# Optimization experiments

Hardware: AMD Instinct MI355X
Metric: run time of the kernel (lower is better)

## Reference

```python
import jax, jax.numpy as jnp
import numpy as np

D_MODEL = 256
D_CONV = 4
EXPAND = 2
D_INNER = EXPAND * D_MODEL  # 512


def silu(v):
    return v * jax.nn.sigmoid(v)


def setup_inputs() -> dict:
    key = jax.random.key(0)
    k0, k1, k2, k3, k4 = jax.random.split(key, 5)
    B, H, W = 4, 128, 128
    x = jax.random.normal(k0, (B, H, W, D_MODEL), jnp.float32)
    # nn.Linear(d_model, 2*d_inner, bias=False) -> weight (2*d_inner, d_model)
    W_in = jax.random.normal(k1, (2 * D_INNER, D_MODEL), jnp.float32) * 0.02
    # depthwise nn.Conv1d(d_inner, d_inner, k=4, groups=d_inner) -> weight (d_inner, 1, k)
    conv_w = jax.random.normal(k2, (D_INNER, 1, D_CONV), jnp.float32) * 0.1
    conv_b = jax.random.normal(k3, (D_INNER,), jnp.float32) * 0.02
    # nn.Linear(d_inner, d_model, bias=False) -> weight (d_model, d_inner)
    W_out = jax.random.normal(k4, (D_MODEL, D_INNER), jnp.float32) * 0.02
    return {"x": x, "W_in": W_in, "conv_w": conv_w, "conv_b": conv_b, "W_out": W_out}


def reference(x, W_in, conv_w, conv_b, W_out):
    B, H, W, C = x.shape
    L = H * W
    x_flat = x.reshape(B, L, C)
    xz = jnp.einsum('blc,dc->bld', x_flat, W_in)         # (B, L, 2*d_inner)
    x_branch, z_branch = jnp.split(xz, 2, axis=-1)
    # depthwise conv1d with padding=d_conv-1 then truncate to L == left-pad by d_conv-1
    u = jax.lax.conv_general_dilated(
        x_branch.transpose(0, 2, 1),                      # (B, D, L)
        conv_w,                                           # (D, 1, K)
        window_strides=(1,),
        padding=[(D_CONV - 1, 0)],
        dimension_numbers=('NCH', 'OIH', 'NCH'),
        feature_group_count=D_INNER,
    )
    u = (u + conv_b[None, :, None]).transpose(0, 2, 1)    # (B, L, D)
    u = silu(u)
    # selective_scan in the source is a stub that returns its input unchanged,
    # so the four directional passes reduce to identity transforms of u.
    y1 = u
    y2 = jnp.flip(jnp.flip(u, axis=1), axis=1)
    u_t = u.reshape(B, H, W, -1).transpose(0, 2, 1, 3).reshape(B, L, -1)
    y3 = u_t.reshape(B, W, H, -1).transpose(0, 2, 1, 3).reshape(B, L, -1)
    y4 = jnp.flip(jnp.flip(u_t, axis=1), axis=1).reshape(B, W, H, -1).transpose(0, 2, 1, 3).reshape(B, L, -1)
    y = (y1 + y2 + y3 + y4) * silu(z_branch)
    out = jnp.einsum('bld,cd->blc', y, W_out)
    return out.reshape(B, H, W, C)
```

## Files before the change

kernel.cpp:

```cpp
#include <hip/hip_runtime.h>

#define LSEQ   16384
#define NBATCH 4
#define BLROWS 65536
#define DM     256
#define DI     512
#define DXZ    1024

#define BM 128
#define BN 128
#define BK 64

typedef __attribute__((ext_vector_type(8))) short s16x8;
typedef __attribute__((ext_vector_type(4))) short s16x4;
typedef __attribute__((ext_vector_type(4))) float f32x4;

__device__ __forceinline__ float bf2f(unsigned short h) {
  union { unsigned u; float f; } c; c.u = ((unsigned)h) << 16; return c.f;
}
__device__ __forceinline__ unsigned short f2bf(float f) {
  union { float f; unsigned u; } c; c.f = f;
  unsigned u = c.u;
  return (unsigned short)((u + 0x7fffu + ((u >> 16) & 1u)) >> 16);
}

__global__ __launch_bounds__(256)
void cvt_f32_bf16(const float* __restrict__ src, unsigned short* __restrict__ dst, int n4) {
  for (int i = blockIdx.x * blockDim.x + threadIdx.x; i < n4; i += gridDim.x * blockDim.x) {
    const float4 v = reinterpret_cast<const float4*>(src)[i];
    s16x4 o;
    o[0] = (short)f2bf(v.x);
    o[1] = (short)f2bf(v.y);
    o[2] = (short)f2bf(v.z);
    o[3] = (short)f2bf(v.w);
    reinterpret_cast<s16x4*>(dst)[i] = o;
  }
}

__device__ __forceinline__ void gload16(const void* g, void* l) {
  __builtin_amdgcn_global_load_lds((__attribute__((address_space(1))) void*)(g),
                                   (__attribute__((address_space(3))) void*)(l),
                                   16, 0, 0);
}

template<int OUT_BF16>
__global__ __launch_bounds__(256, 2)
void gemm_bt(const unsigned short* __restrict__ A,
             const unsigned short* __restrict__ B,
             void* __restrict__ Cv,
             int M, int N, int K) {
  __shared__ unsigned short lds[2][BM * BK + BN * BK];

  const int tid  = threadIdx.x;
  const int lane = tid & 63;
  const int wv   = tid >> 6;
  const int wr   = wv >> 1;
  const int wc   = wv & 1;
  const int m0   = blockIdx.y * BM;
  const int n0   = blockIdx.x * BN;

  const int srow = tid >> 3;
  const int scol = (tid & 7) * 8;

  const int kSteps = K / BK;

  f32x4 acc[4][4];
#pragma unroll
  for (int i = 0; i < 4; ++i)
#pragma unroll
    for (int j = 0; j < 4; ++j)
#pragma unroll
      for (int r = 0; r < 4; ++r) acc[i][j][r] = 0.f;

  auto stage = [&](int ks, int buf) {
    const unsigned short* Ag = A + (size_t)(m0 + srow) * K + ks * BK + scol;
    const unsigned short* Bg = B + (size_t)(n0 + srow) * K + ks * BK + scol;
    unsigned short* lA = &lds[buf][0]       + tid * 8;
    unsigned short* lB = &lds[buf][BM * BK] + tid * 8;
#pragma unroll
    for (int i = 0; i < 4; ++i) {
      gload16(Ag + (size_t)(i * 32) * K, lA + i * 2048);
      gload16(Bg + (size_t)(i * 32) * K, lB + i * 2048);
    }
  };

  stage(0, 0);

  for (int ks = 0; ks < kSteps; ++ks) {
    const int cur = ks & 1;
    __syncthreads();
    if (ks + 1 < kSteps) stage(ks + 1, cur ^ 1);

    const unsigned short* lA = &lds[cur][0];
    const unsigned short* lB = &lds[cur][BM * BK];
    const int lrow = lane & 15;
#pragma unroll
    for (int kk = 0; kk < BK; kk += 32) {
      const int lk = kk + ((lane >> 4) << 3);
      s16x8 af[4], bf[4];
#pragma unroll
      for (int i = 0; i < 4; ++i)
        af[i] = *(const s16x8*)(lA + (wr * 64 + i * 16 + lrow) * BK + lk);
#pragma unroll
      for (int j = 0; j < 4; ++j)
        bf[j] = *(const s16x8*)(lB + (wc * 64 + j * 16 + lrow) * BK + lk);
#pragma unroll
      for (int i = 0; i < 4; ++i)
#pragma unroll
        for (int j = 0; j < 4; ++j)
          acc[i][j] = __builtin_amdgcn_mfma_f32_16x16x32_bf16(af[i], bf[j], acc[i][j], 0, 0, 0);
    }
  }

  const int r0 = (lane >> 4) * 4;
  const int c0 = lane & 15;
  if (OUT_BF16) {
    unsigned short* C = (unsigned short*)Cv;
#pragma unroll
    for (int i = 0; i < 4; ++i)
#pragma unroll
      for (int j = 0; j < 4; ++j) {
        const int rr = m0 + wr * 64 + i * 16 + r0;
        const int cc = n0 + wc * 64 + j * 16 + c0;
#pragma unroll
        for (int r = 0; r < 4; ++r)
          C[(size_t)(rr + r) * N + cc] = f2bf(acc[i][j][r]);
      }
  } else {
    float* C = (float*)Cv;
#pragma unroll
    for (int i = 0; i < 4; ++i)
#pragma unroll
      for (int j = 0; j < 4; ++j) {
        const int rr = m0 + wr * 64 + i * 16 + r0;
        const int cc = n0 + wc * 64 + j * 16 + c0;
#pragma unroll
        for (int r = 0; r < 4; ++r)
          C[(size_t)(rr + r) * N + cc] = acc[i][j][r];
      }
  }
}

__global__ __launch_bounds__(256)
void conv_gate(const unsigned short* __restrict__ xz,
               const float* __restrict__ cw,
               const float* __restrict__ cb,
               unsigned short* __restrict__ y) {
  const int tid      = threadIdx.x;
  const int rowLocal = tid >> 6;
  const int row      = blockIdx.x * 4 + rowLocal;
  const int l        = row & (LSEQ - 1);
  const int d0       = (tid & 63) * 8;
  const size_t base  = (size_t)row * DXZ;

  s16x8 t[4];
#pragma unroll
  for (int k = 0; k < 4; ++k) {
    const int lp = l - 3 + k;
    if (lp >= 0) {
      t[k] = *(const s16x8*)(xz + base + (long)(k - 3) * (long)DXZ + d0);
    } else {
#pragma unroll
      for (int j = 0; j < 8; ++j) t[k][j] = 0;
    }
  }
  const s16x8 zv = *(const s16x8*)(xz + base + DI + d0);

  s16x8 o;
#pragma unroll
  for (int j = 0; j < 8; ++j) {
    const float4 wj = *(const float4*)(cw + (size_t)(d0 + j) * 4);
    float a = cb[d0 + j];
    a += wj.x * bf2f((unsigned short)t[0][j]);
    a += wj.y * bf2f((unsigned short)t[1][j]);
    a += wj.z * bf2f((unsigned short)t[2][j]);
    a += wj.w * bf2f((unsigned short)t[3][j]);
    const float su = a / (1.f + __expf(-a));
    const float zf = bf2f((unsigned short)zv[j]);
    const float sz = zf / (1.f + __expf(-zf));
    o[j] = (short)f2bf(4.f * su * sz);
  }
  *(s16x8*)(y + (size_t)row * DI + d0) = o;
}

extern "C" void kernel_launch(void* const* d_in, const int* in_sizes, int n_in,
                              void* d_out, int out_size, void* d_ws, size_t ws_size,
                              hipStream_t stream) {
  const float* x      = (const float*)d_in[0];
  const float* W_in   = (const float*)d_in[1];
  const float* conv_w = (const float*)d_in[2];
  const float* conv_b = (const float*)d_in[3];
  const float* W_out  = (const float*)d_in[4];

  char* ws = (char*)d_ws;
  unsigned short* x_bf   = (unsigned short*)(ws);
  unsigned short* y_bf   = (unsigned short*)(ws);
  unsigned short* xz_bf  = (unsigned short*)(ws + 67108864ull);
  unsigned short* win_bf = (unsigned short*)(ws + 201326592ull);
  unsigned short* wout_bf= (unsigned short*)(ws + 201850880ull);

  cvt_f32_bf16<<<2048, 256, 0, stream>>>(x,      x_bf,    (BLROWS * DM) / 4);
  cvt_f32_bf16<<<256,  256, 0, stream>>>(W_in,   win_bf,  (DXZ * DM) / 4);
  cvt_f32_bf16<<<128,  256, 0, stream>>>(W_out,  wout_bf, (DM * DI) / 4);

  gemm_bt<1><<<dim3(DXZ / BN, BLROWS / BM), 256, 0, stream>>>(
      x_bf, win_bf, xz_bf, BLROWS, DXZ, DM);

  conv_gate<<<BLROWS / 4, 256, 0, stream>>>(xz_bf, conv_w, conv_b, y_bf);

  gemm_bt<0><<<dim3(DM / BN, BLROWS / BM), 256, 0, stream>>>(
      y_bf, wout_bf, d_out, BLROWS, DM, DI);
}
```

Measured before the change: 297.9 us.

## Fuse input GEMM with depthwise conv and SiLU gating, eliminating xz buffer

The first GEMM now computes paired x-branch and z-branch column tiles for the same channels in one block. It writes them into swizzled LDS and applies the causal depthwise conv, bias, and SiLU gating in the epilogue. The three-row halo preceding each tile is recomputed with scalar dot products. This removes the bf16 xz intermediate write/read and a kernel launch, at the cost of a heavier epilogue and redundant halo compute. The SiLU divisions also switch to fast reciprocals.

```diff
diff --git a/kernel.cpp b/kernel.cpp
--- a/kernel.cpp
+++ b/kernel.cpp
@@ -1,7 +1,6 @@
 #include <hip/hip_runtime.h>
 
 #define LSEQ   16384
-#define NBATCH 4
 #define BLROWS 65536
 #define DM     256
 #define DI     512
@@ -43,12 +42,162 @@
                                    16, 0, 0);
 }
 
-template<int OUT_BF16>
+__device__ __forceinline__ int xswz(int row, int byteInRow) {
+  return row * 128 + (byteInRow ^ ((row & 7) << 4));
+}
+
 __global__ __launch_bounds__(256, 2)
-void gemm_bt(const unsigned short* __restrict__ A,
-             const unsigned short* __restrict__ B,
-             void* __restrict__ Cv,
-             int M, int N, int K) {
+void gemm1_conv(const unsigned short* __restrict__ A,
+                const unsigned short* __restrict__ Bw,
+                const float* __restrict__ cw,
+                const float* __restrict__ cb,
+                unsigned short* __restrict__ Y) {
+  __shared__ unsigned short lds[2][BM * BK + BN * BK];
+
+  const int tid  = threadIdx.x;
+  const int lane = tid & 63;
+  const int wv   = tid >> 6;
+  const int wr   = wv >> 1;
+  const int wc   = wv & 1;
+  const int m0   = blockIdx.y * BM;
+  const int n0x  = blockIdx.x * 64;
+
+  const int srow = tid >> 3;
+  const int scol = (tid & 7) * 8;
+
+  f32x4 acc[4][4];
+#pragma unroll
+  for (int i = 0; i < 4; ++i)
+#pragma unroll
+    for (int j = 0; j < 4; ++j)
+#pragma unroll
+      for (int r = 0; r < 4; ++r) acc[i][j][r] = 0.f;
+
+  auto stage = [&](int ks, int buf) {
+    const unsigned short* Ag = A + (size_t)(m0 + srow) * DM + ks * BK + scol;
+    unsigned short* lA = &lds[buf][0]       + tid * 8;
+    unsigned short* lB = &lds[buf][BM * BK] + tid * 8;
+#pragma unroll
+    for (int i = 0; i < 4; ++i) {
+      gload16(Ag + (size_t)(i * 32) * DM, lA + i * 2048);
+      const int lr   = srow + i * 32;
+      const int grow = (i < 2) ? (n0x + lr) : (448 + n0x + lr);
+      gload16(Bw + (size_t)grow * DM + ks * BK + scol, lB + i * 2048);
+    }
+  };
+
+  stage(0, 0);
+
+  const int kSteps = DM / BK;
+  for (int ks = 0; ks < kSteps; ++ks) {
+    const int cur = ks & 1;
+    __syncthreads();
+    if (ks + 1 < kSteps) stage(ks + 1, cur ^ 1);
+
+    const unsigned short* lA = &lds[cur][0];
+    const unsigned short* lB = &lds[cur][BM * BK];
+    const int lrow = lane & 15;
+#pragma unroll
+    for (int kk = 0; kk < BK; kk += 32) {
+      const int lk = kk + ((lane >> 4) << 3);
+      s16x8 af[4], bf[4];
+#pragma unroll
+      for (int i = 0; i < 4; ++i)
+        af[i] = *(const s16x8*)(lA + (wr * 64 + i * 16 + lrow) * BK + lk);
+#pragma unroll
+      for (int j = 0; j < 4; ++j)
+        bf[j] = *(const s16x8*)(lB + (wc * 64 + j * 16 + lrow) * BK + lk);
+#pragma unroll
+      for (int i = 0; i < 4; ++i)
+#pragma unroll
+        for (int j = 0; j < 4; ++j)
+          acc[i][j] = __builtin_amdgcn_mfma_f32_16x16x32_bf16(af[i], bf[j], acc[i][j], 0, 0, 0);
+    }
+  }
+
+  __syncthreads();
+  char* ldsb = (char*)&lds[0][0];
+  const int r0 = (lane >> 4) * 4;
+  const int c0 = lane & 15;
+
+  if (wc == 0) {
+#pragma unroll
+    for (int i = 0; i < 4; ++i)
+#pragma unroll
+      for (int j = 0; j < 4; ++j)
+#pragma unroll
+        for (int r = 0; r < 4; ++r) {
+          const int row = wr * 64 + i * 16 + r0 + r;
+          const int col = j * 16 + c0;
+          *(unsigned short*)(ldsb + xswz(row + 3, col * 2)) = f2bf(acc[i][j][r]);
+        }
+  } else {
+#pragma unroll
+    for (int i = 0; i < 4; ++i)
+#pragma unroll
+      for (int j = 0; j < 4; ++j)
+#pragma unroll
+        for (int r = 0; r < 4; ++r) {
+          const int row = wr * 64 + i * 16 + r0 + r;
+          const int col = j * 16 + c0;
+          *(unsigned short*)(ldsb + 16768 + xswz(row, col * 2)) = f2bf(acc[i][j][r]);
+        }
+  }
+
+  if (tid < 192) {
+    const int hi = tid >> 6;
+    const int hc = tid & 63;
+    float s = 0.f;
+    if ((m0 & (LSEQ - 1)) != 0) {
+      const unsigned short* xr = A  + (size_t)(m0 - 3 + hi) * DM;
+      const unsigned short* wr_ = Bw + (size_t)(n0x + hc) * DM;
+#pragma unroll
+      for (int kk = 0; kk < DM; kk += 8) {
+        const s16x8 xa = *(const s16x8*)(xr + kk);
+        const s16x8 wa = *(const s16x8*)(wr_ + kk);
+#pragma unroll
+        for (int j = 0; j < 8; ++j)
+          s += bf2f((unsigned short)xa[j]) * bf2f((unsigned short)wa[j]);
+      }
+    }
+    *(unsigned short*)(ldsb + xswz(hi, hc * 2)) = f2bf(s);
+  }
+  __syncthreads();
+
+  const int rr2 = tid >> 1;
+  const int cb2 = (tid & 1) * 32;
+#pragma unroll
+  for (int v = 0; v < 4; ++v) {
+    const int c = cb2 + v * 8;
+    const s16x8 t0 = *(const s16x8*)(ldsb + xswz(rr2 + 0, c * 2));
+    const s16x8 t1 = *(const s16x8*)(ldsb + xswz(rr2 + 1, c * 2));
+    const s16x8 t2 = *(const s16x8*)(ldsb + xswz(rr2 + 2, c * 2));
+    const s16x8 t3 = *(const s16x8*)(ldsb + xswz(rr2 + 3, c * 2));
+    const s16x8 zv = *(const s16x8*)(ldsb + 16768 + xswz(rr2, c * 2));
+    s16x8 o;
+#pragma unroll
+    for (int j = 0; j < 8; ++j) {
+      const int ch = n0x + c + j;
+      const float4 w4 = *(const float4*)(cw + (size_t)ch * 4);
+      float a = cb[ch];
+      a += w4.x * bf2f((unsigned short)t0[j]);
+      a += w4.y * bf2f((unsigned short)t1[j]);
+      a += w4.z * bf2f((unsigned short)t2[j]);
+      a += w4.w * bf2f((unsigned short)t3[j]);
+      const float su = a * __builtin_amdgcn_rcpf(1.f + __expf(-a));
+      const float z  = bf2f((unsigned short)zv[j]);
+      const float sz = z * __builtin_amdgcn_rcpf(1.f + __expf(-z));
+      o[j] = (short)f2bf(4.f * su * sz);
+    }
+    *(s16x8*)(Y + (size_t)(m0 + rr2) * DI + n0x + c) = o;
+  }
+}
+
+__global__ __launch_bounds__(256, 2)
+void gemm_bt_f32(const unsigned short* __restrict__ A,
+                 const unsigned short* __restrict__ B,
+                 float* __restrict__ C,
+                 int M, int N, int K) {
   __shared__ unsigned short lds[2][BM * BK + BN * BK];
 
   const int tid  = threadIdx.x;
@@ -114,73 +263,16 @@
 
   const int r0 = (lane >> 4) * 4;
   const int c0 = lane & 15;
-  if (OUT_BF16) {
-    unsigned short* C = (unsigned short*)Cv;
-#pragma unroll
-    for (int i = 0; i < 4; ++i)
-#pragma unroll
-      for (int j = 0; j < 4; ++j) {
-        const int rr = m0 + wr * 64 + i * 16 + r0;
-        const int cc = n0 + wc * 64 + j * 16 + c0;
-#pragma unroll
-        for (int r = 0; r < 4; ++r)
-          C[(size_t)(rr + r) * N + cc] = f2bf(acc[i][j][r]);
-      }
-  } else {
-    float* C = (float*)Cv;
-#pragma unroll
-    for (int i = 0; i < 4; ++i)
-#pragma unroll
-      for (int j = 0; j < 4; ++j) {
-        const int rr = m0 + wr * 64 + i * 16 + r0;
-        const int cc = n0 + wc * 64 + j * 16 + c0;
-#pragma unroll
-        for (int r = 0; r < 4; ++r)
-          C[(size_t)(rr + r) * N + cc] = acc[i][j][r];
-      }
-  }
-}
-
-__global__ __launch_bounds__(256)
-void conv_gate(const unsigned short* __restrict__ xz,
-               const float* __restrict__ cw,
-               const float* __restrict__ cb,
-               unsigned short* __restrict__ y) {
-  const int tid      = threadIdx.x;
-  const int rowLocal = tid >> 6;
-  const int row      = blockIdx.x * 4 + rowLocal;
-  const int l        = row & (LSEQ - 1);
-  const int d0       = (tid & 63) * 8;
-  const size_t base  = (size_t)row * DXZ;
-
-  s16x8 t[4];
-#pragma unroll
-  for (int k = 0; k < 4; ++k) {
-    const int lp = l - 3 + k;
-    if (lp >= 0) {
-      t[k] = *(const s16x8*)(xz + base + (long)(k - 3) * (long)DXZ + d0);
-    } else {
-#pragma unroll
-      for (int j = 0; j < 8; ++j) t[k][j] = 0;
-    }
-  }
-  const s16x8 zv = *(const s16x8*)(xz + base + DI + d0);
-
-  s16x8 o;
-#pragma unroll
-  for (int j = 0; j < 8; ++j) {
-    const float4 wj = *(const float4*)(cw + (size_t)(d0 + j) * 4);
-    float a = cb[d0 + j];
-    a += wj.x * bf2f((unsigned short)t[0][j]);
-    a += wj.y * bf2f((unsigned short)t[1][j]);
-    a += wj.z * bf2f((unsigned short)t[2][j]);
-    a += wj.w * bf2f((unsigned short)t[3][j]);
-    const float su = a / (1.f + __expf(-a));
-    const float zf = bf2f((unsigned short)zv[j]);
-    const float sz = zf / (1.f + __expf(-zf));
-    o[j] = (short)f2bf(4.f * su * sz);
-  }
-  *(s16x8*)(y + (size_t)row * DI + d0) = o;
+#pragma unroll
+  for (int i = 0; i < 4; ++i)
+#pragma unroll
+    for (int j = 0; j < 4; ++j) {
+      const int rr = m0 + wr * 64 + i * 16 + r0;
+      const int cc = n0 + wc * 64 + j * 16 + c0;
+#pragma unroll
+      for (int r = 0; r < 4; ++r)
+        C[(size_t)(rr + r) * N + cc] = acc[i][j][r];
+    }
 }
 
 extern "C" void kernel_launch(void* const* d_in, const int* in_sizes, int n_in,
@@ -193,21 +285,18 @@
   const float* W_out  = (const float*)d_in[4];
 
   char* ws = (char*)d_ws;
-  unsigned short* x_bf   = (unsigned short*)(ws);
-  unsigned short* y_bf   = (unsigned short*)(ws);
-  unsigned short* xz_bf  = (unsigned short*)(ws + 67108864ull);
-  unsigned short* win_bf = (unsigned short*)(ws + 201326592ull);
-  unsigned short* wout_bf= (unsigned short*)(ws + 201850880ull);
-
-  cvt_f32_bf16<<<2048, 256, 0, stream>>>(x,      x_bf,    (BLROWS * DM) / 4);
-  cvt_f32_bf16<<<256,  256, 0, stream>>>(W_in,   win_bf,  (DXZ * DM) / 4);
-  cvt_f32_bf16<<<128,  256, 0, stream>>>(W_out,  wout_bf, (DM * DI) / 4);
-
-  gemm_bt<1><<<dim3(DXZ / BN, BLROWS / BM), 256, 0, stream>>>(
-      x_bf, win_bf, xz_bf, BLROWS, DXZ, DM);
-
-  conv_gate<<<BLROWS / 4, 256, 0, stream>>>(xz_bf, conv_w, conv_b, y_bf);
-
-  gemm_bt<0><<<dim3(DM / BN, BLROWS / BM), 256, 0, stream>>>(
-      y_bf, wout_bf, d_out, BLROWS, DM, DI);
-}
+  unsigned short* y_bf    = (unsigned short*)(ws);
+  unsigned short* x_bf    = (unsigned short*)(ws + (64ull << 20));
+  unsigned short* win_bf  = (unsigned short*)(ws + (100ull << 20));
+  unsigned short* wout_bf = (unsigned short*)(ws + (101ull << 20));
+
+  cvt_f32_bf16<<<2048, 256, 0, stream>>>(x,     x_bf,    (BLROWS * DM) / 4);
+  cvt_f32_bf16<<<256,  256, 0, stream>>>(W_in,  win_bf,  (DXZ * DM) / 4);
+  cvt_f32_bf16<<<128,  256, 0, stream>>>(W_out, wout_bf, (DM * DI) / 4);
+
+  gemm1_conv<<<dim3(DI / 64, BLROWS / BM), 256, 0, stream>>>(
+      x_bf, win_bf, conv_w, conv_b, y_bf);
+
+  gemm_bt_f32<<<dim3(DM / BN, BLROWS / BM), 256, 0, stream>>>(
+      y_bf, wout_bf, (float*)d_out, BLROWS, DM, DI);
+}
```

New measurement: 307.0 us. 3.1% more time.
